# Optimization experiments

Hardware: AMD Instinct MI355X
Metric: run time of the kernel (lower is better)

## Reference

```python
import jax, jax.numpy as jnp
import numpy as np

B = 8
GXN, GYN = 240, 121  # internal lon/lat grid sizes


def nearest_resize(x, oh, ow):
    # torch F.interpolate mode='nearest' on NCHW: idx = floor(i * in/out)
    H, W = x.shape[2], x.shape[3]
    hi = (jnp.arange(oh) * H) // oh
    wi = (jnp.arange(ow) * W) // ow
    return x[:, :, hi][:, :, :, wi]


def _kern(p, g, ls):
    # p: (B,N), g: (G,) -> (B,N,G) RBF weights
    d = p[:, :, None] - g[None, None, :]
    return jnp.exp(-0.5 * d * d / (ls * ls))


def setconv_off_to_on(px, py, y, gx, gy, ls, eps=1e-6):
    # Off-grid points -> grid. px,py: (B,N); y: (B,C,N).
    fin = jnp.isfinite(y)
    m = fin.astype(y.dtype)
    yv = jnp.where(fin, y, 0.0)
    kx = _kern(px, gx, ls)  # (B,N,Gx)
    ky = _kern(py, gy, ls)  # (B,N,Gy)

    def per_ch(args):
        mc, yc = args  # (B,N) each
        den = jnp.einsum('bni,bnj->bij', kx * mc[:, :, None], ky)
        sig = jnp.einsum('bni,bnj->bij', kx * yc[:, :, None], ky)
        return den, sig

    den, sig = jax.lax.map(per_ch, (jnp.swapaxes(m, 0, 1), jnp.swapaxes(yv, 0, 1)))
    den = jnp.swapaxes(den, 0, 1)  # (B,C,Gx,Gy)
    sig = jnp.swapaxes(sig, 0, 1) / (den + eps)
    Bb, C = y.shape[0], y.shape[1]
    return jnp.stack([den, sig], axis=2).reshape(Bb, 2 * C, gx.shape[0], gy.shape[0])


def setconv_on_to_on(xlon, xlat, w, gx, gy, ls, eps=1e-6):
    # Source grid -> internal grid, separable RBF. xlon:(B,H), xlat:(B,W), w:(B,C,H,W).
    fin = jnp.isfinite(w)
    m = fin.astype(w.dtype)
    wv = jnp.where(fin, w, 0.0)
    kx = _kern(xlon, gx, ls)  # (B,H,Gx)
    ky = _kern(xlat, gy, ls)  # (B,W,Gy)
    den = jnp.einsum('bchw,bhi,bwj->bcij', m, kx, ky)
    sig = jnp.einsum('bchw,bhi,bwj->bcij', wv, kx, ky) / (den + eps)
    Bb, C = w.shape[0], w.shape[1]
    return jnp.stack([den, sig], axis=2).reshape(Bb, 2 * C, gx.shape[0], gy.shape[0])


def _forward(iasi_current, ascat_current, hadisd_x, hadisd_y, icoads_x, icoads_current, sat_x_lon, sat_x_lat, sat_current, amsua_x_lon, amsua_x_lat, amsua_current, amsub_x_lon, amsub_x_lat, amsub_current, hirs_x_lon, hirs_x_lat, hirs_current, igra_x, igra_current, era5_elev, climatology, aux_time, ls):
    lsv = ls[0]
    gx = (jnp.linspace(0.0, 360.0, GXN) / 360.0).astype(jnp.float32)
    gy = (jnp.linspace(-90.0, 90.0, GYN) / 360.0).astype(jnp.float32)
    enc = []
    # IASI / ASCAT: nan->0, nearest interp to (240,121), flip lat axis
    e = nearest_resize(jnp.transpose(jnp.nan_to_num(iasi_current), (0, 3, 1, 2)), GXN, GYN)
    enc.append(jnp.flip(e, axis=-1))
    e = nearest_resize(jnp.transpose(jnp.nan_to_num(ascat_current), (0, 3, 1, 2)), GXN, GYN)
    enc.append(jnp.flip(e, axis=-1))
    # HadISD: 4 off-grid channels
    had = [setconv_off_to_on(hadisd_x[c, :, 0], hadisd_x[c, :, 1], hadisd_y[c][:, None, :], gx, gy, lsv) for c in range(4)]
    enc.append(jnp.concatenate(had, axis=1))
    # ICOADS: 5 off-grid channels (shared point cloud)
    enc.append(setconv_off_to_on(icoads_x[:, 0], icoads_x[:, 1], icoads_current, gx, gy, lsv))
    # GRIDSAT: 2 on-grid channels
    enc.append(setconv_on_to_on(sat_x_lon, sat_x_lat, sat_current, gx, gy, lsv))
    # AMSU-A: last channel nan'd, zeros nan'd, permute(0,3,2,1)
    w = jnp.transpose(amsua_current, (0, 3, 2, 1))  # (B,13,240,121)
    w = w.at[:, -1].set(jnp.nan)
    w = jnp.where(w == 0.0, jnp.nan, w)
    enc.append(setconv_on_to_on(amsua_x_lon, amsua_x_lat, w, gx, gy, lsv))
    # AMSU-B: zeros nan'd, permute(0,3,1,2)
    w = jnp.transpose(amsub_current, (0, 3, 1, 2))
    w = jnp.where(w == 0.0, jnp.nan, w)
    enc.append(setconv_on_to_on(amsub_x_lon, amsub_x_lat, w, gx, gy, lsv))
    # IGRA: 24 off-grid channels
    enc.append(setconv_off_to_on(igra_x[:, 0], igra_x[:, 1], igra_current, gx, gy, lsv))
    # HIRS: 26 on-grid channels
    w = jnp.transpose(hirs_current, (0, 3, 1, 2))
    w = jnp.where(w == 0.0, jnp.nan, w)
    enc.append(setconv_on_to_on(hirs_x_lon, hirs_x_lat, w, gx, gy, lsv))
    # Elevation: permute, flip, nearest interp to internal grid
    el = jnp.flip(jnp.transpose(era5_elev, (0, 1, 3, 2)), axis=2)
    el = nearest_resize(el, GYN, GXN)  # (B,1,121,240)
    enc.append(jnp.transpose(el, (0, 1, 3, 2)))  # align to (B,1,240,121)
    enc.append(climatology)
    enc.append(jnp.ones_like(climatology[:, :1]) * aux_time[:, :, None, None])
    x = jnp.concatenate(enc, axis=1)  # (B,213,240,121)
    return x


def setup_inputs() -> dict:
    key = jax.random.key(0)
    ks = jax.random.split(key, 24)
    f32 = jnp.float32
    d = {}
    d['iasi_current'] = jax.random.normal(ks[0], (B, 120, 60, 8), f32)
    d['ascat_current'] = jax.random.normal(ks[1], (B, 120, 60, 3), f32)
    hx = jax.random.uniform(ks[2], (4, B, 2, 5000), f32)
    d['hadisd_x'] = hx.at[:, :, 1].set(hx[:, :, 1] * 0.5 - 0.25)
    d['hadisd_y'] = jax.random.normal(ks[3], (4, B, 5000), f32)
    ix = jax.random.uniform(ks[4], (B, 2, 20000), f32)
    d['icoads_x'] = ix.at[:, 1].set(ix[:, 1] * 0.5 - 0.25)
    d['icoads_current'] = jax.random.normal(ks[5], (B, 5, 20000), f32)
    d['sat_x_lon'] = jnp.sort(jax.random.uniform(ks[6], (B, 360), f32), axis=-1)
    d['sat_x_lat'] = jnp.sort(jax.random.uniform(ks[7], (B, 180), f32) * 0.5 - 0.25, axis=-1)
    d['sat_current'] = jax.random.normal(ks[8], (B, 2, 360, 180), f32)
    d['amsua_x_lon'] = jnp.sort(jax.random.uniform(ks[9], (B, 240), f32), axis=-1)
    d['amsua_x_lat'] = jnp.sort(jax.random.uniform(ks[10], (B, 121), f32) * 0.5 - 0.25, axis=-1)
    d['amsua_current'] = jax.random.normal(ks[11], (B, 121, 240, 13), f32)
    d['amsub_x_lon'] = jnp.sort(jax.random.uniform(ks[12], (B, 240), f32), axis=-1)
    d['amsub_x_lat'] = jnp.sort(jax.random.uniform(ks[13], (B, 121), f32) * 0.5 - 0.25, axis=-1)
    d['amsub_current'] = jax.random.normal(ks[14], (B, 240, 121, 12), f32)
    d['hirs_x_lon'] = jnp.sort(jax.random.uniform(ks[15], (B, 240), f32), axis=-1)
    d['hirs_x_lat'] = jnp.sort(jax.random.uniform(ks[16], (B, 121), f32) * 0.5 - 0.25, axis=-1)
    d['hirs_current'] = jax.random.normal(ks[17], (B, 240, 121, 26), f32)
    gxp = jax.random.uniform(ks[18], (B, 2, 3000), f32)
    d['igra_x'] = gxp.at[:, 1].set(gxp[:, 1] * 0.5 - 0.25)
    d['igra_current'] = jax.random.normal(ks[19], (B, 24, 3000), f32)
    d['era5_elev'] = jax.random.normal(ks[20], (B, 1, 480, 242), f32)
    d['climatology'] = jax.random.normal(ks[21], (B, 24, 240, 121), f32)
    d['aux_time'] = jax.random.normal(ks[22], (B, 5), f32)
    d['ls'] = jnp.full((1,), 0.001, f32)  # learned RBF lengthscale (init 0.001)
    return d


def reference(iasi_current, ascat_current, hadisd_x, hadisd_y, icoads_x, icoads_current, sat_x_lon, sat_x_lat, sat_current, amsua_x_lon, amsua_x_lat, amsua_current, amsub_x_lon, amsub_x_lat, amsub_current, hirs_x_lon, hirs_x_lat, hirs_current, igra_x, igra_current, era5_elev, climatology, aux_time, ls):
    return _forward(iasi_current, ascat_current, hadisd_x, hadisd_y, icoads_x, icoads_current, sat_x_lon, sat_x_lat, sat_current, amsua_x_lon, amsua_x_lat, amsua_current, amsub_x_lon, amsub_x_lat, amsub_current, hirs_x_lon, hirs_x_lat, hirs_current, igra_x, igra_current, era5_elev, climatology, aux_time, ls)
```

## Files before the change

### kernel.cpp

```cpp
#include <hip/hip_runtime.h>
#include <cmath>

#define GXN 240
#define GYN 121
#define SP  29040
#define NB  8
#define NCH 213
#define EPSV 1e-6f
#define DMAXF 7.75f
#define ACLIP -30.0f

#define P_HAD   160000
#define P_ICO   160000
#define P_IGRA  24000
#define PT_TOT  344000
#define VB_TOT  48
#define NCELL   (VB_TOT*SP)
#define CBLK    908
#define NGROUP  39

__device__ __forceinline__ float gxv(int i){ return (float)i * (1.0f/239.0f); }
__device__ __forceinline__ float gyv(int j){ return -0.25f + (float)j * (1.0f/240.0f); }
__device__ __forceinline__ size_t oidx(int b,int c,int i,int j){
  return (((size_t)b*NCH + c)*GXN + i)*GYN + j;
}
__device__ __forceinline__ int binx(float x){
  int i = (int)floorf(x*239.0f + 0.5f);
  return i<0?0:(i>239?239:i);
}
__device__ __forceinline__ int biny(float y){
  int j = (int)floorf((y+0.25f)*240.0f + 0.5f);
  return j<0?0:(j>120?120:j);
}
__device__ __forceinline__ int lbnd(const float* a, int n, float v){
  int lo=0, hi=n;
  while(lo<hi){ int m=(lo+hi)>>1; if(a[m]<v) lo=m+1; else hi=m; }
  return lo;
}
__device__ __forceinline__ int ubnd(const float* a, int n, float v){
  int lo=0, hi=n;
  while(lo<hi){ int m=(lo+hi)>>1; if(a[m]<=v) lo=m+1; else hi=m; }
  return lo;
}

struct PtLoc { int ds, vb, n; float x, y; };
__device__ __forceinline__ PtLoc ptloc(int idx, const float* hadx, const float* icx, const float* igx){
  PtLoc p;
  if(idx < P_HAD){
    p.ds=0; p.vb=idx/5000; p.n=idx%5000;
    p.x = hadx[(size_t)p.vb*10000 + p.n];
    p.y = hadx[(size_t)p.vb*10000 + 5000 + p.n];
  } else if(idx < P_HAD + P_ICO){
    int t = idx - P_HAD; p.ds=1; p.vb=t/20000; p.n=t%20000;
    p.x = icx[(size_t)p.vb*40000 + p.n];
    p.y = icx[(size_t)p.vb*40000 + 20000 + p.n];
  } else {
    int t = idx - (P_HAD+P_ICO); p.ds=2; p.vb=t/3000; p.n=t%3000;
    p.x = igx[(size_t)p.vb*6000 + p.n];
    p.y = igx[(size_t)p.vb*6000 + 3000 + p.n];
  }
  return p;
}
__device__ __forceinline__ int vbglobal(const PtLoc& p){
  return (p.ds==0)? p.vb : (p.ds==1? 32+p.vb : 40+p.vb);
}

__global__ void kzero_i(int* __restrict__ p, int n){
  int i = blockIdx.x*blockDim.x + threadIdx.x;
  if(i<n) p[i]=0;
}

__global__ void kcount(const float* __restrict__ hadx, const float* __restrict__ icx,
                       const float* __restrict__ igx, int* __restrict__ counts){
  int idx = blockIdx.x*blockDim.x + threadIdx.x;
  if(idx >= PT_TOT) return;
  PtLoc p = ptloc(idx, hadx, icx, igx);
  atomicAdd(counts + vbglobal(p)*SP + binx(p.x)*GYN + biny(p.y), 1);
}

__global__ void kscan1(const int* __restrict__ in, int* __restrict__ part,
                       int* __restrict__ bsum, int n){
  __shared__ int ts[256];
  int t = threadIdx.x;
  int base = blockIdx.x*1024 + t*4;
  int v0=0,v1=0,v2=0,v3=0;
  if(base+0<n) v0=in[base+0];
  if(base+1<n) v1=in[base+1];
  if(base+2<n) v2=in[base+2];
  if(base+3<n) v3=in[base+3];
  ts[t]=v0+v1+v2+v3; __syncthreads();
  for(int off=1; off<256; off<<=1){
    int x = (t>=off)? ts[t-off] : 0; __syncthreads();
    ts[t]+=x; __syncthreads();
  }
  int ex = (t==0)? 0 : ts[t-1];
  if(base+0<n) part[base+0]=ex;
  if(base+1<n) part[base+1]=ex+v0;
  if(base+2<n) part[base+2]=ex+v0+v1;
  if(base+3<n) part[base+3]=ex+v0+v1+v2;
  if(t==255) bsum[blockIdx.x]=ts[255];
}

__global__ void kscan2(int* __restrict__ b, int n){
  __shared__ int ts[256];
  int t = threadIdx.x;
  int v[16]; int s=0;
#pragma unroll
  for(int k=0;k<16;k++){ int p=t*16+k; v[k] = (p<n)? b[p] : 0; s+=v[k]; }
  ts[t]=s; __syncthreads();
  for(int off=1; off<256; off<<=1){
    int x = (t>=off)? ts[t-off] : 0; __syncthreads();
    ts[t]+=x; __syncthreads();
  }
  int run = (t==0)? 0 : ts[t-1];
#pragma unroll
  for(int k=0;k<16;k++){ int p=t*16+k; if(p<n) b[p]=run; run+=v[k]; }
}

__global__ void kscan3(const int* __restrict__ part, const int* __restrict__ bsum,
                       int* __restrict__ offs, int* __restrict__ cursor, int n){
  int i = blockIdx.x*blockDim.x + threadIdx.x;
  if(i==0) offs[n] = PT_TOT;
  if(i>=n) return;
  int v = part[i] + bsum[i>>10];
  offs[i]=v; cursor[i]=v;
}

__global__ void kpack(const float* __restrict__ hadx, const float* __restrict__ icx,
                      const float* __restrict__ igx,
                      const float* __restrict__ hady, const float* __restrict__ icy,
                      const float* __restrict__ igy,
                      int* __restrict__ cursor,
                      float* __restrict__ had_rec, float* __restrict__ ico_rec,
                      float* __restrict__ igra_rec){
  int idx = blockIdx.x*blockDim.x + threadIdx.x;
  if(idx >= PT_TOT) return;
  PtLoc p = ptloc(idx, hadx, icx, igx);
  int cell = vbglobal(p)*SP + binx(p.x)*GYN + biny(p.y);
  int pos = atomicAdd(cursor + cell, 1);
  if(p.ds==0){
    float* r = had_rec + (size_t)pos*4;
    r[0]=p.x; r[1]=p.y;
    r[2]=hady[(size_t)p.vb*5000 + p.n];
  } else if(p.ds==1){
    float* r = ico_rec + (size_t)(pos - P_HAD)*8;
    r[0]=p.x; r[1]=p.y;
#pragma unroll
    for(int c=0;c<5;c++) r[2+c]=icy[((size_t)p.vb*5 + c)*20000 + p.n];
  } else {
    float* r = igra_rec + (size_t)(pos - P_HAD - P_ICO)*28;
    r[0]=p.x; r[1]=p.y;
#pragma unroll
    for(int c=0;c<24;c++) r[2+c]=igy[((size_t)p.vb*24 + c)*3000 + p.n];
  }
}

__device__ __forceinline__ void copy_one(int cc, int b, int i, int j,
    const float* __restrict__ iasi, const float* __restrict__ ascat,
    const float* __restrict__ elev, const float* __restrict__ clim,
    const float* __restrict__ aux, float* __restrict__ out){
  float v; int oc;
  if(cc < 8){
    int hi = i>>1, wi = ((120 - j)*60)/121;
    v = iasi[((b*120 + hi)*60 + wi)*8 + cc];
    if(!isfinite(v)) v = isnan(v) ? 0.f : (v>0.f? 3.4028235e38f : -3.4028235e38f);
    oc = cc;
  } else if(cc < 11){
    int hi = i>>1, wi = ((120 - j)*60)/121;
    v = ascat[((b*120 + hi)*60 + wi)*3 + (cc-8)];
    if(!isfinite(v)) v = isnan(v) ? 0.f : (v>0.f? 3.4028235e38f : -3.4028235e38f);
    oc = cc;
  } else if(cc == 11){
    v = elev[(b*480 + 2*i)*242 + (241 - 2*j)];
    oc = 183;
  } else if(cc < 36){
    int c = cc-12;
    v = clim[(((size_t)b*24 + c)*GXN + i)*GYN + j];
    oc = 184 + c;
  } else {
    v = aux[b*5 + (cc-36)];
    oc = 208 + (cc-36);
  }
  out[oidx(b,oc,i,j)] = v;
}

__device__ __forceinline__ void ongrid(const float* __restrict__ lon, const float* __restrict__ lat,
    const float* __restrict__ base, int H, int W, int sH, int sW, int sC,
    int c0, int cg, int maskedC, bool zmask, int chOut,
    float inv2, float dmax, int b, int i, int j, float* __restrict__ out){
  float gi = gxv(i), gj = gyv(j);
  int hlo = lbnd(lon,H,gi-dmax), hhi = ubnd(lon,H,gi+dmax);
  int wlo = lbnd(lat,W,gj-dmax), whi = ubnd(lat,W,gj+dmax);
  float den[4]={0.f,0.f,0.f,0.f}, sig[4]={0.f,0.f,0.f,0.f};
  for(int h=hlo; h<hhi; h++){
    float dx = lon[h]-gi;
    float ax = -dx*dx*inv2;
    if(ax < ACLIP) continue;
    const float* rowp = base + (size_t)h*sH + (size_t)c0*sC;
    for(int w=wlo; w<whi; w++){
      float dy = lat[w]-gj;
      float a = ax - dy*dy*inv2;
      if(a < ACLIP) continue;
      float wt = expf(a);
      const float* s = rowp + (size_t)w*sW;
#pragma unroll
      for(int c=0;c<4;c++){
        if(c<cg){
          float v = s[c*sC];
          bool ok = isfinite(v);
          if(zmask) ok = ok && (v!=0.0f);
          if(c0+c == maskedC) ok = false;
          if(ok){ den[c]+=wt; sig[c]+=wt*v; }
        }
      }
    }
  }
#pragma unroll
  for(int c=0;c<4;c++){
    if(c<cg){
      size_t d = oidx(b, chOut + 2*c, i, j);
      out[d]    = den[c];
      out[d+SP] = sig[c]/(den[c]+EPSV);
    }
  }
}

__device__ __forceinline__ void offgrid(const float* __restrict__ rec, int RS,
    const int* __restrict__ offs, int dsBase, int vbG, int voff, int cg, int chOut,
    float inv2, float dmax, int b, int i, int j, float* __restrict__ out){
  int rbx = (int)floorf(dmax*239.0f + 0.5f);
  int rby = (int)floorf(dmax*240.0f + 0.5f);
  float gi = gxv(i), gj = gyv(j);
  int ilo = i-rbx; if(ilo<0) ilo=0;
  int ihi = i+rbx; if(ihi>GXN-1) ihi=GXN-1;
  int jlo = j-rby; if(jlo<0) jlo=0;
  int jhi = j+rby; if(jhi>GYN-1) jhi=GYN-1;
  int jspan = jhi - jlo;
  float den[4]={0.f,0.f,0.f,0.f}, sig[4]={0.f,0.f,0.f,0.f};
  for(int bi=ilo; bi<=ihi; bi++){
    int cb0 = vbG*SP + bi*GYN + jlo;
    int s = offs[cb0] - dsBase;
    int e = offs[cb0 + jspan + 1] - dsBase;
    for(int t=s; t<e; t++){
      const float* r = rec + (size_t)t*RS;
      float dx = r[0]-gi, dy = r[1]-gj;
      float a = -(dx*dx + dy*dy)*inv2;
      if(a < ACLIP) continue;
      float wt = expf(a);
#pragma unroll
      for(int c=0;c<4;c++){
        if(c<cg){
          float v = r[voff+c];
          if(isfinite(v)){ den[c]+=wt; sig[c]+=wt*v; }
        }
      }
    }
  }
#pragma unroll
  for(int c=0;c<4;c++){
    if(c<cg){
      size_t d = oidx(b, chOut + 2*c, i, j);
      out[d]    = den[c];
      out[d+SP] = sig[c]/(den[c]+EPSV);
    }
  }
}

__global__ __launch_bounds__(256) void kmega(
    const float* __restrict__ iasi, const float* __restrict__ ascat,
    const float* __restrict__ elev, const float* __restrict__ clim,
    const float* __restrict__ aux,
    const float* __restrict__ slon, const float* __restrict__ slat, const float* __restrict__ scur,
    const float* __restrict__ alon, const float* __restrict__ alat, const float* __restrict__ acur,
    const float* __restrict__ blon, const float* __restrict__ blat, const float* __restrict__ bcur,
    const float* __restrict__ hlon, const float* __restrict__ hlat, const float* __restrict__ hcur,
    const float* __restrict__ had_rec, const float* __restrict__ ico_rec,
    const float* __restrict__ igra_rec, const int* __restrict__ offs,
    const float* __restrict__ lsp, float* __restrict__ out){
  int g = blockIdx.x / CBLK;
  int t = (blockIdx.x % CBLK)*blockDim.x + threadIdx.x;
  if(t >= NB*SP) return;
  int j = t%GYN; int i = (t/GYN)%GXN; int b = t/SP;
  float ls = lsp[0];
  float inv2 = 0.5f/(ls*ls);
  float dmax = DMAXF*ls;

  if(g < 11){
    int cb = g*4;
#pragma unroll
    for(int k=0;k<4;k++){
      int cc = cb+k;
      if(cc < 41) copy_one(cc, b, i, j, iasi, ascat, elev, clim, aux, out);
    }
  } else if(g < 13){
    int c0 = g-11;
    ongrid(slon + b*360, slat + b*180, scur + (size_t)b*2*360*180,
           360, 180, 180, 1, 64800, c0, 1, -1, false, 29 + 2*c0,
           inv2, dmax, b, i, j, out);
  } else if(g < 17){
    int c0 = (g-13)*4;
    int cg = 13-c0 < 4 ? 13-c0 : 4;
    ongrid(alon + b*240, alat + b*121, acur + (size_t)b*121*240*13,
           240, 121, 13, 3120, 1, c0, cg, 12, true, 33 + 2*c0,
           inv2, dmax, b, i, j, out);
  } else if(g < 20){
    int c0 = (g-17)*4;
    ongrid(blon + b*240, blat + b*121, bcur + (size_t)b*240*121*12,
           240, 121, 1452, 12, 1, c0, 4, -1, true, 59 + 2*c0,
           inv2, dmax, b, i, j, out);
  } else if(g < 27){
    int c0 = (g-20)*4;
    int cg = 26-c0 < 4 ? 26-c0 : 4;
    ongrid(hlon + b*240, hlat + b*121, hcur + (size_t)b*240*121*26,
           240, 121, 3146, 26, 1, c0, cg, -1, true, 131 + 2*c0,
           inv2, dmax, b, i, j, out);
  } else if(g < 31){
    int set = g-27;
    offgrid(had_rec, 4, offs, 0, set*8 + b, 2, 1, 11 + 2*set,
            inv2, dmax, b, i, j, out);
  } else if(g < 33){
    int c0 = (g-31)*4;
    int cg = 5-c0 < 4 ? 5-c0 : 4;
    offgrid(ico_rec, 8, offs, P_HAD, 32 + b, 2 + c0, cg, 19 + 2*c0,
            inv2, dmax, b, i, j, out);
  } else {
    int c0 = (g-33)*4;
    offgrid(igra_rec, 28, offs, P_HAD + P_ICO, 40 + b, 2 + c0, 4, 83 + 2*c0,
            inv2, dmax, b, i, j, out);
  }
}

extern "C" void kernel_launch(void* const* d_in, const int* in_sizes, int n_in,
                              void* d_out, int out_size, void* d_ws, size_t ws_size,
                              hipStream_t stream){
  const float* iasi  = (const float*)d_in[0];
  const float* ascat = (const float*)d_in[1];
  const float* hadx  = (const float*)d_in[2];
  const float* hady  = (const float*)d_in[3];
  const float* icx   = (const float*)d_in[4];
  const float* icy   = (const float*)d_in[5];
  const float* slon  = (const float*)d_in[6];
  const float* slat  = (const float*)d_in[7];
  const float* scur  = (const float*)d_in[8];
  const float* alon  = (const float*)d_in[9];
  const float* alat  = (const float*)d_in[10];
  const float* acur  = (const float*)d_in[11];
  const float* blon  = (const float*)d_in[12];
  const float* blat  = (const float*)d_in[13];
  const float* bcur  = (const float*)d_in[14];
  const float* hlon  = (const float*)d_in[15];
  const float* hlat  = (const float*)d_in[16];
  const float* hcur  = (const float*)d_in[17];
  const float* igx   = (const float*)d_in[18];
  const float* igy   = (const float*)d_in[19];
  const float* elev  = (const float*)d_in[20];
  const float* clim  = (const float*)d_in[21];
  const float* aux   = (const float*)d_in[22];
  const float* ls    = (const float*)d_in[23];
  float* out = (float*)d_out;
  dim3 tb(256);
  auto nb = [](long long n){ return dim3((unsigned)((n+255)/256)); };

  int* counts = (int*)d_ws;
  int* offs   = counts + NCELL;
  int* bsum   = offs + NCELL + 1;
  float* had_rec  = (float*)(bsum + 4096);
  float* ico_rec  = had_rec + 640000;
  float* igra_rec = ico_rec + 1280000;

  int nblk = (NCELL + 1023)/1024;

  kzero_i<<<nb(NCELL),tb,0,stream>>>(counts, NCELL);
  kcount <<<nb(PT_TOT),tb,0,stream>>>(hadx, icx, igx, counts);
  kscan1 <<<dim3(nblk),tb,0,stream>>>(counts, offs, bsum, NCELL);
  kscan2 <<<dim3(1),tb,0,stream>>>(bsum, nblk);
  kscan3 <<<nb(NCELL),tb,0,stream>>>(offs, bsum, offs, counts, NCELL);
  kpack  <<<nb(PT_TOT),tb,0,stream>>>(hadx, icx, igx, hady, icy, igy,
                                      counts, had_rec, ico_rec, igra_rec);

  kmega<<<dim3(NGROUP*CBLK),tb,0,stream>>>(iasi, ascat, elev, clim, aux,
      slon, slat, scur, alon, alat, acur, blon, blat, bcur, hlon, hlat, hcur,
      had_rec, ico_rec, igra_rec, offs, ls, out);
}
```

Measured before the change: 805.1 us.

## Split on-grid setconv into row-per-block kernel with LDS-staged source rows

Moves the on-grid (sat/amsua/amsub/hirs) RBF accumulation into a new kernel where each block handles one output row (b,i). Each source row h is staged in shared memory and all channels are accumulated per thread, instead of recomputing weights per 4-channel group. It also transposes the amsua input to channel-last in a separate kernel and repacks the off-grid records into compact 6-float per-group layouts to cut strided loads. Risks: only 121 of 128 threads are active, there is a __syncthreads per source row, and the extra transpose pass and workspace add traffic.

```diff
diff --git a/kernel.cpp b/kernel.cpp
--- a/kernel.cpp
+++ b/kernel.cpp
@@ -17,7 +17,7 @@
 #define VB_TOT  48
 #define NCELL   (VB_TOT*SP)
 #define CBLK    908
-#define NGROUP  39
+#define NGOFF   23
 
 __device__ __forceinline__ float gxv(int i){ return (float)i * (1.0f/239.0f); }
 __device__ __forceinline__ float gyv(int j){ return -0.25f + (float)j * (1.0f/240.0f); }
@@ -143,15 +143,120 @@
     r[0]=p.x; r[1]=p.y;
     r[2]=hady[(size_t)p.vb*5000 + p.n];
   } else if(p.ds==1){
-    float* r = ico_rec + (size_t)(pos - P_HAD)*8;
-    r[0]=p.x; r[1]=p.y;
-#pragma unroll
-    for(int c=0;c<5;c++) r[2+c]=icy[((size_t)p.vb*5 + c)*20000 + p.n];
+    int lp = pos - P_HAD;
+    float* r0 = ico_rec + (size_t)lp*6;
+    r0[0]=p.x; r0[1]=p.y;
+#pragma unroll
+    for(int c=0;c<4;c++) r0[2+c]=icy[((size_t)p.vb*5 + c)*20000 + p.n];
+    float* r1 = ico_rec + 960000 + (size_t)lp*6;
+    r1[0]=p.x; r1[1]=p.y;
+    r1[2]=icy[((size_t)p.vb*5 + 4)*20000 + p.n];
   } else {
-    float* r = igra_rec + (size_t)(pos - P_HAD - P_ICO)*28;
-    r[0]=p.x; r[1]=p.y;
-#pragma unroll
-    for(int c=0;c<24;c++) r[2+c]=igy[((size_t)p.vb*24 + c)*3000 + p.n];
+    int lp = pos - P_HAD - P_ICO;
+#pragma unroll
+    for(int g=0; g<6; g++){
+      float* r = igra_rec + (size_t)g*144000 + (size_t)lp*6;
+      r[0]=p.x; r[1]=p.y;
+#pragma unroll
+      for(int k=0;k<4;k++) r[2+k]=igy[((size_t)p.vb*24 + g*4 + k)*3000 + p.n];
+    }
+  }
+}
+
+__global__ void ktransA(const float* __restrict__ acur, float* __restrict__ planeA){
+  int idx = blockIdx.x*blockDim.x + threadIdx.x;
+  if(idx >= NB*121*240*13) return;
+  int c = idx%13; int h=(idx/13)%240; int w=(idx/3120)%121; int b=idx/377520;
+  planeA[(((size_t)b*240 + h)*121 + w)*13 + c] = acur[idx];
+}
+
+template<int C, bool CHLAST>
+__device__ __forceinline__ void ongrid_row(
+    const float* __restrict__ lon, int H,
+    const float* __restrict__ lat, int W,
+    const float* __restrict__ src, size_t sH, size_t sW, size_t sC,
+    int maskedC, bool zmask, int chOut,
+    float inv2, float dmax, int b, int i,
+    float* __restrict__ out, float* __restrict__ lds)
+{
+  float gi = gxv(i);
+  int hlo = lbnd(lon,H,gi-dmax), hhi = ubnd(lon,H,gi+dmax);
+  int j = threadIdx.x;
+  bool act = j < GYN;
+  float gj = gyv(act? j : 0);
+  int wlo=0, whi=0;
+  if(act){ wlo = lbnd(lat,W,gj-dmax); whi = ubnd(lat,W,gj+dmax); }
+  float den[C], sig[C];
+#pragma unroll
+  for(int c=0;c<C;c++){ den[c]=0.f; sig[c]=0.f; }
+  for(int h=hlo; h<hhi; h++){
+    __syncthreads();
+    const float* rp = src + (size_t)h*sH;
+    if(CHLAST){
+      for(int t=threadIdx.x; t<W*C; t+=blockDim.x) lds[t] = rp[t];
+    } else {
+      for(int t=threadIdx.x; t<W*C; t+=blockDim.x){
+        int w=t/C, c=t%C;
+        lds[t] = rp[(size_t)w*sW + (size_t)c*sC];
+      }
+    }
+    __syncthreads();
+    if(!act) continue;
+    float dx = lon[h]-gi;
+    float ax = -dx*dx*inv2;
+    if(ax < ACLIP) continue;
+    for(int w=wlo; w<whi; w++){
+      float dy = lat[w]-gj;
+      float a = ax - dy*dy*inv2;
+      if(a < ACLIP) continue;
+      float wt = expf(a);
+      const float* s = lds + w*C;
+#pragma unroll
+      for(int c=0;c<C;c++){
+        float v = s[c];
+        bool ok = isfinite(v);
+        if(zmask) ok = ok && (v!=0.0f);
+        if(c==maskedC) ok = false;
+        if(ok){ den[c]+=wt; sig[c]+=wt*v; }
+      }
+    }
+  }
+  if(act){
+#pragma unroll
+    for(int c=0;c<C;c++){
+      size_t d = oidx(b, chOut+2*c, i, j);
+      out[d]    = den[c];
+      out[d+SP] = sig[c]/(den[c]+EPSV);
+    }
+  }
+}
+
+__global__ __launch_bounds__(128) void kongrid(
+    const float* __restrict__ slon, const float* __restrict__ slat, const float* __restrict__ scur,
+    const float* __restrict__ alon, const float* __restrict__ alat, const float* __restrict__ planeA,
+    const float* __restrict__ blon, const float* __restrict__ blat, const float* __restrict__ bcur,
+    const float* __restrict__ hlon, const float* __restrict__ hlat, const float* __restrict__ hcur,
+    const float* __restrict__ lsp, float* __restrict__ out)
+{
+  __shared__ float lds[3146];
+  int blk = blockIdx.x;
+  int ds = blk / 1920, r = blk % 1920;
+  int b = r/240, i = r%240;
+  float ls = lsp[0];
+  float inv2 = 0.5f/(ls*ls);
+  float dmax = DMAXF*ls;
+  if(ds==0){
+    ongrid_row<2,false>(slon+b*360,360, slat+b*180,180,
+      scur + (size_t)b*129600, 180,1,64800, -1,false, 29, inv2,dmax,b,i,out,lds);
+  } else if(ds==1){
+    ongrid_row<13,true>(alon+b*240,240, alat+b*121,121,
+      planeA + (size_t)b*377520, 1573,13,1, 12,true, 33, inv2,dmax,b,i,out,lds);
+  } else if(ds==2){
+    ongrid_row<12,true>(blon+b*240,240, blat+b*121,121,
+      bcur + (size_t)b*348480, 1452,12,1, -1,true, 59, inv2,dmax,b,i,out,lds);
+  } else {
+    ongrid_row<26,true>(hlon+b*240,240, hlat+b*121,121,
+      hcur + (size_t)b*755040, 3146,26,1, -1,true, 131, inv2,dmax,b,i,out,lds);
   }
 }
 
@@ -184,49 +289,8 @@
   out[oidx(b,oc,i,j)] = v;
 }
 
-__device__ __forceinline__ void ongrid(const float* __restrict__ lon, const float* __restrict__ lat,
-    const float* __restrict__ base, int H, int W, int sH, int sW, int sC,
-    int c0, int cg, int maskedC, bool zmask, int chOut,
-    float inv2, float dmax, int b, int i, int j, float* __restrict__ out){
-  float gi = gxv(i), gj = gyv(j);
-  int hlo = lbnd(lon,H,gi-dmax), hhi = ubnd(lon,H,gi+dmax);
-  int wlo = lbnd(lat,W,gj-dmax), whi = ubnd(lat,W,gj+dmax);
-  float den[4]={0.f,0.f,0.f,0.f}, sig[4]={0.f,0.f,0.f,0.f};
-  for(int h=hlo; h<hhi; h++){
-    float dx = lon[h]-gi;
-    float ax = -dx*dx*inv2;
-    if(ax < ACLIP) continue;
-    const float* rowp = base + (size_t)h*sH + (size_t)c0*sC;
-    for(int w=wlo; w<whi; w++){
-      float dy = lat[w]-gj;
-      float a = ax - dy*dy*inv2;
-      if(a < ACLIP) continue;
-      float wt = expf(a);
-      const float* s = rowp + (size_t)w*sW;
-#pragma unroll
-      for(int c=0;c<4;c++){
-        if(c<cg){
-          float v = s[c*sC];
-          bool ok = isfinite(v);
-          if(zmask) ok = ok && (v!=0.0f);
-          if(c0+c == maskedC) ok = false;
-          if(ok){ den[c]+=wt; sig[c]+=wt*v; }
-        }
-      }
-    }
-  }
-#pragma unroll
-  for(int c=0;c<4;c++){
-    if(c<cg){
-      size_t d = oidx(b, chOut + 2*c, i, j);
-      out[d]    = den[c];
-      out[d+SP] = sig[c]/(den[c]+EPSV);
-    }
-  }
-}
-
 __device__ __forceinline__ void offgrid(const float* __restrict__ rec, int RS,
-    const int* __restrict__ offs, int dsBase, int vbG, int voff, int cg, int chOut,
+    const int* __restrict__ offs, int dsBase, int vbG, int cg, int chOut,
     float inv2, float dmax, int b, int i, int j, float* __restrict__ out){
   int rbx = (int)floorf(dmax*239.0f + 0.5f);
   int rby = (int)floorf(dmax*240.0f + 0.5f);
@@ -250,7 +314,7 @@
 #pragma unroll
       for(int c=0;c<4;c++){
         if(c<cg){
-          float v = r[voff+c];
+          float v = r[2+c];
           if(isfinite(v)){ den[c]+=wt; sig[c]+=wt*v; }
         }
       }
@@ -266,14 +330,10 @@
   }
 }
 
-__global__ __launch_bounds__(256) void kmega(
+__global__ __launch_bounds__(256) void kmoff(
     const float* __restrict__ iasi, const float* __restrict__ ascat,
     const float* __restrict__ elev, const float* __restrict__ clim,
     const float* __restrict__ aux,
-    const float* __restrict__ slon, const float* __restrict__ slat, const float* __restrict__ scur,
-    const float* __restrict__ alon, const float* __restrict__ alat, const float* __restrict__ acur,
-    const float* __restrict__ blon, const float* __restrict__ blat, const float* __restrict__ bcur,
-    const float* __restrict__ hlon, const float* __restrict__ hlat, const float* __restrict__ hcur,
     const float* __restrict__ had_rec, const float* __restrict__ ico_rec,
     const float* __restrict__ igra_rec, const int* __restrict__ offs,
     const float* __restrict__ lsp, float* __restrict__ out){
@@ -292,41 +352,18 @@
       int cc = cb+k;
       if(cc < 41) copy_one(cc, b, i, j, iasi, ascat, elev, clim, aux, out);
     }
-  } else if(g < 13){
-    int c0 = g-11;
-    ongrid(slon + b*360, slat + b*180, scur + (size_t)b*2*360*180,
-           360, 180, 180, 1, 64800, c0, 1, -1, false, 29 + 2*c0,
-           inv2, dmax, b, i, j, out);
+  } else if(g < 15){
+    int set = g-11;
+    offgrid(had_rec, 4, offs, 0, set*8 + b, 1, 11 + 2*set,
+            inv2, dmax, b, i, j, out);
   } else if(g < 17){
-    int c0 = (g-13)*4;
-    int cg = 13-c0 < 4 ? 13-c0 : 4;
-    ongrid(alon + b*240, alat + b*121, acur + (size_t)b*121*240*13,
-           240, 121, 13, 3120, 1, c0, cg, 12, true, 33 + 2*c0,
-           inv2, dmax, b, i, j, out);
-  } else if(g < 20){
-    int c0 = (g-17)*4;
-    ongrid(blon + b*240, blat + b*121, bcur + (size_t)b*240*121*12,
-           240, 121, 1452, 12, 1, c0, 4, -1, true, 59 + 2*c0,
-           inv2, dmax, b, i, j, out);
-  } else if(g < 27){
-    int c0 = (g-20)*4;
-    int cg = 26-c0 < 4 ? 26-c0 : 4;
-    ongrid(hlon + b*240, hlat + b*121, hcur + (size_t)b*240*121*26,
-           240, 121, 3146, 26, 1, c0, cg, -1, true, 131 + 2*c0,
-           inv2, dmax, b, i, j, out);
-  } else if(g < 31){
-    int set = g-27;
-    offgrid(had_rec, 4, offs, 0, set*8 + b, 2, 1, 11 + 2*set,
-            inv2, dmax, b, i, j, out);
-  } else if(g < 33){
-    int c0 = (g-31)*4;
-    int cg = 5-c0 < 4 ? 5-c0 : 4;
-    offgrid(ico_rec, 8, offs, P_HAD, 32 + b, 2 + c0, cg, 19 + 2*c0,
-            inv2, dmax, b, i, j, out);
+    int grp = g-15;
+    offgrid(ico_rec + (size_t)grp*960000, 6, offs, P_HAD, 32 + b,
+            grp==0?4:1, 19 + 8*grp, inv2, dmax, b, i, j, out);
   } else {
-    int c0 = (g-33)*4;
-    offgrid(igra_rec, 28, offs, P_HAD + P_ICO, 40 + b, 2 + c0, 4, 83 + 2*c0,
-            inv2, dmax, b, i, j, out);
+    int grp = g-17;
+    offgrid(igra_rec + (size_t)grp*144000, 6, offs, P_HAD + P_ICO, 40 + b,
+            4, 83 + 8*grp, inv2, dmax, b, i, j, out);
   }
 }
 
@@ -366,9 +403,12 @@
   int* bsum   = offs + NCELL + 1;
   float* had_rec  = (float*)(bsum + 4096);
   float* ico_rec  = had_rec + 640000;
-  float* igra_rec = ico_rec + 1280000;
+  float* igra_rec = ico_rec + 1920000;
+  float* planeA   = igra_rec + 864000;
 
   int nblk = (NCELL + 1023)/1024;
+
+  ktransA<<<nb((long long)NB*121*240*13),tb,0,stream>>>(acur, planeA);
 
   kzero_i<<<nb(NCELL),tb,0,stream>>>(counts, NCELL);
   kcount <<<nb(PT_TOT),tb,0,stream>>>(hadx, icx, igx, counts);
@@ -378,7 +418,9 @@
   kpack  <<<nb(PT_TOT),tb,0,stream>>>(hadx, icx, igx, hady, icy, igy,
                                       counts, had_rec, ico_rec, igra_rec);
 
-  kmega<<<dim3(NGROUP*CBLK),tb,0,stream>>>(iasi, ascat, elev, clim, aux,
-      slon, slat, scur, alon, alat, acur, blon, blat, bcur, hlon, hlat, hcur,
+  kongrid<<<dim3(4*1920),dim3(128),0,stream>>>(slon, slat, scur,
+      alon, alat, planeA, blon, blat, bcur, hlon, hlat, hcur, ls, out);
+
+  kmoff<<<dim3(NGOFF*CBLK),tb,0,stream>>>(iasi, ascat, elev, clim, aux,
       had_rec, ico_rec, igra_rec, offs, ls, out);
 }
```

Result: faster. 694.6 us (-13.7%).
